# Kernel optimization log

Measured on AMD Instinct MI355X. Metric: run time of the kernel, lower is better.

## Reference

```python
import jax, jax.numpy as jnp
import numpy as np


def setup_inputs() -> dict:
    key = jax.random.key(0)
    ks = jax.random.split(key, 6)
    b, c, h, w = 8, 256, 48, 48
    return {
        "qry_fts": jax.random.normal(ks[0], (b, c, h, w), dtype=jnp.float32),
        "mask_fts": jax.random.normal(ks[1], (b, c, h, w), dtype=jnp.float32),
        "fts": jax.random.normal(ks[2], (b, c, h, w), dtype=jnp.float32),
        "Wq": jax.random.normal(ks[3], (c, c), dtype=jnp.float32) * (1.0 / np.sqrt(c)),
        "Wk": jax.random.normal(ks[4], (c, c), dtype=jnp.float32) * (1.0 / np.sqrt(c)),
        "Wv": jax.random.normal(ks[5], (c, c), dtype=jnp.float32) * (1.0 / np.sqrt(c)),
        "mu": jnp.full((1,), 0.5, dtype=jnp.float32),
    }


def reference(qry_fts, mask_fts, fts, Wq, Wk, Wv, mu):
    b, c, h, w = qry_fts.shape
    # flatten spatial dims to tokens: [b, N, c], N = h*w
    q_tok = qry_fts.reshape(b, c, h * w).transpose(0, 2, 1)
    m_tok = mask_fts.reshape(b, c, h * w).transpose(0, 2, 1)
    f_tok = fts.reshape(b, c, h * w).transpose(0, 2, 1)

    # torch Linear(no bias): y = x @ W^T with W [out,in]
    Q = jnp.einsum("bnc,dc->bnd", q_tok, Wq)
    K1 = jnp.einsum("bnc,dc->bnd", f_tok, Wk)
    K2 = jnp.einsum("bnc,dc->bnd", m_tok, Wk)
    V = jnp.einsum("bnc,dc->bnd", f_tok, Wv)

    A1 = jax.nn.softmax(jnp.einsum("bqd,bkd->bqk", Q, K1), axis=-1)
    A2 = jax.nn.softmax(jnp.einsum("bqd,bkd->bqk", Q, K2), axis=-1)
    A = (A1 * 0.5 + A2 * mu[0]) / (0.5 + mu[0])

    att = jnp.einsum("bqk,bkd->bqd", A, V)  # [b, N, c]
    att = att.reshape(b, h, w, c).transpose(0, 3, 1, 2)
    return qry_fts + att
```

## Files before the change

kernel.cpp:

```cpp
#include <hip/hip_runtime.h>
#include <math.h>

#define BB 8
#define CC 256
#define NTOK 2304
#define NPL 36
#define LOG2E 1.4426950408889634f
#define BIAS2 72.134752f

typedef __attribute__((ext_vector_type(4))) float f32x4;
typedef __attribute__((ext_vector_type(8))) short s16x8;
typedef __attribute__((ext_vector_type(4))) short s16x4;

__device__ inline unsigned short f2bf(float x) {
  unsigned u = __builtin_bit_cast(unsigned, x);
  return (unsigned short)((u + 0x7FFFu + ((u >> 16) & 1u)) >> 16);
}
__device__ inline float bf2f(unsigned short h) {
  return __builtin_bit_cast(float, (unsigned)h << 16);
}
__device__ inline unsigned short f2h(float x) {
  _Float16 h = (_Float16)x;
  return __builtin_bit_cast(unsigned short, h);
}

__device__ inline void async16(void* lds, const void* g) {
  __builtin_amdgcn_global_load_lds(
      (const __attribute__((address_space(1))) unsigned int*)g,
      (__attribute__((address_space(3))) unsigned int*)lds, 16, 0, 0);
}

__global__ __launch_bounds__(256)
void prep_kernel(const float* __restrict__ X0, const float* __restrict__ X1,
                 const float* __restrict__ X2, unsigned short* __restrict__ Y0,
                 unsigned short* __restrict__ Y1, unsigned short* __restrict__ Y2) {
  __shared__ float Ls[64][65];
  const int t = threadIdx.x;
  const int n0 = blockIdx.x * 64, c0 = blockIdx.y * 64;
  const int z = blockIdx.z, src = z >> 3, b = z & 7;
  const float* X = (src == 0) ? X0 : (src == 1) ? X1 : X2;
  unsigned short* Y = (src == 0) ? Y0 : (src == 1) ? Y1 : Y2;
  const float* Xb = X + (size_t)b * CC * NTOK;
  unsigned short* Yb = Y + (size_t)b * CC * NTOK;

  #pragma unroll
  for (int rr = 0; rr < 16; rr++) {
    int cl = rr * 4 + (t >> 6);
    Ls[cl][t & 63] = Xb[(size_t)(c0 + cl) * NTOK + n0 + (t & 63)];
  }
  __syncthreads();
  #pragma unroll
  for (int rr = 0; rr < 8; rr++) {
    int nl = rr * 8 + (t >> 5);
    int cl = (t & 31) * 2;
    unsigned v = (unsigned)f2h(Ls[cl][nl]) | ((unsigned)f2h(Ls[cl + 1][nl]) << 16);
    *(unsigned*)((char*)Yb + ((size_t)(n0 + nl) * CC + c0 + cl) * 2) = v;
  }
}

__global__ __launch_bounds__(256)
void wconv_kernel(const float* __restrict__ Wq, const float* __restrict__ Wk,
                  const float* __restrict__ Wv, unsigned short* __restrict__ Wqh,
                  unsigned short* __restrict__ Wkh, unsigned short* __restrict__ Wvh) {
  const float* src = (blockIdx.y == 0) ? Wq : (blockIdx.y == 1) ? Wk : Wv;
  unsigned short* dst = (blockIdx.y == 0) ? Wqh : (blockIdx.y == 1) ? Wkh : Wvh;
  int gi = (blockIdx.x * 256 + threadIdx.x) * 4;
  f32x4 v = *(const f32x4*)(src + gi);
  s16x4 o;
  #pragma unroll
  for (int i = 0; i < 4; i++) o[i] = (short)f2h(v[i]);
  *(s16x4*)(dst + gi) = o;
}

template<int MODE>
__global__ __launch_bounds__(256, 2)
void gemm_kernel(const unsigned short* __restrict__ Xt, const unsigned short* __restrict__ Wh,
                 unsigned short* __restrict__ Y) {
  __shared__ alignas(16) char smem[32768];

  const int t = threadIdx.x;
  const int w = t >> 6, l = t & 63, g = l >> 4, c = l & 15;
  const int bid = blockIdx.x;
  const int b = bid & 7, nt = bid >> 3;
  const int n0w = nt * 64 + w * 16;
  const size_t bo = (size_t)b * CC * NTOK;

  const char* Xb = (const char*)(Xt + bo);
  const char* Wb = (const char*)Wh;
  char* Yb = (char*)(Y + bo);

  int koff[4], cdst[4];
  #pragma unroll
  for (int j = 0; j < 4; j++) {
    int ck = w + 4 * j;
    int row = ck * 2 + (l >> 5);
    koff[j] = row * 512 + (((l & 31) * 16) ^ ((row & 7) << 4));
    cdst[j] = ck * 1024 + l * 16;
  }
  int kxor[8];
  #pragma unroll
  for (int dc = 0; dc < 8; dc++)
    kxor[dc] = (dc * 64 + g * 16) ^ ((c & 7) << 4);

  s16x8 xa[8];
  #pragma unroll
  for (int dc = 0; dc < 8; dc++)
    xa[dc] = *(const s16x8*)(Xb + (n0w + c) * 512 + dc * 64 + g * 16);

  f32x4 acc[16];

#define STAGE_W(WB, TILE)                                            \
  do {                                                               \
    _Pragma("unroll")                                                \
    for (int j_ = 0; j_ < 4; j_++)                                   \
      async16((WB) + cdst[j_], Wb + (TILE) * 16384 + koff[j_]);      \
  } while (0)

  STAGE_W(smem, 0);
  __syncthreads();

  #pragma unroll
  for (int ph = 0; ph < 8; ph++) {
    char* cur = smem + (ph & 1) * 16384;
    if (ph < 7) STAGE_W(smem + ((ph & 1) ^ 1) * 16384, ph + 1);
    __builtin_amdgcn_s_setprio(1);
    #pragma unroll
    for (int s = 0; s < 2; s++) {
      const char* Kt = cur + (s * 16 + c) * 512;
      f32x4 sx[2] = {(f32x4){0.f, 0.f, 0.f, 0.f}, (f32x4){0.f, 0.f, 0.f, 0.f}};
      #pragma unroll
      for (int dc = 0; dc < 8; dc++) {
        s16x8 wf = *(const s16x8*)(Kt + kxor[dc]);
        sx[dc >> 2] = __builtin_amdgcn_mfma_f32_16x16x32_f16(xa[dc], wf, sx[dc >> 2], 0, 0, 0);
      }
      acc[ph * 2 + s] = sx[0] + sx[1];
    }
    __builtin_amdgcn_s_setprio(0);
    __syncthreads();
  }
#undef STAGE_W

  if (MODE == 0 || MODE == 1) {
    unsigned short* Ws = (unsigned short*)(smem + w * 8192);
    #pragma unroll
    for (int dt = 0; dt < 16; dt++)
      #pragma unroll
      for (int j = 0; j < 4; j++) {
        float v = (MODE == 0) ? acc[dt][j] * LOG2E : acc[dt][j];
        Ws[(g * 4 + j) * 256 + dt * 16 + c] = f2h(v);
      }
    #pragma unroll
    for (int r = 0; r < 16; r++) {
      s16x4 v = *(const s16x4*)&Ws[r * 256 + l * 4];
      *(s16x4*)(Yb + (size_t)(n0w + r) * 512 + l * 8) = v;
    }
  } else {
    unsigned short* Vs = (unsigned short*)(smem + w * 8192);
    #pragma unroll
    for (int dt = 0; dt < 16; dt++) {
      s16x4 pv;
      #pragma unroll
      for (int j = 0; j < 4; j++) pv[j] = (short)f2bf(acc[dt][j]);
      *(s16x4*)&Vs[c * 20 + g * 4] = pv;
      s16x4 vv = *(const s16x4*)&Vs[(l >> 2) * 20 + (l & 3) * 4];
      *(s16x4*)(Yb + (size_t)(dt * 16 + (l >> 2)) * 4608 + (size_t)(n0w + (l & 3) * 4) * 2) = vv;
    }
  }
}

__global__ __launch_bounds__(256, 2)
void attn_kernel(const unsigned short* __restrict__ Qf, const unsigned short* __restrict__ K1,
                 const unsigned short* __restrict__ K2, const unsigned short* __restrict__ Vt,
                 unsigned short* __restrict__ pa1, unsigned short* __restrict__ pa2,
                 float* __restrict__ lb) {
  __shared__ alignas(16) char smem[74752];
  char* const kb0 = smem;
  char* const kb1 = smem + 16384;

  const int t = threadIdx.x;
  const int w = t >> 6, l = t & 63, g = l >> 4, c = l & 15;
  const int bid = blockIdx.x;
  const int b = bid & 7;
  const int r0 = bid >> 3;
  const int qt = r0 % 36, half = r0 / 36;
  const int q0 = qt * 64 + w * 16;
  const size_t bo = (size_t)b * CC * NTOK;

  const char* Qb  = (const char*)(Qf + bo);
  const char* K1b = (const char*)(K1 + bo);
  const char* K2b = (const char*)(K2 + bo);
  const char* Vtb = (const char*)(Vt + bo);

  unsigned short* const Pe0 = (unsigned short*)(smem + 65536 + w * 2304);
  unsigned short* const Pe1 = Pe0 + 384;
  unsigned short* const Pod = Pe0 + 768;

  int koff[2], voff[2], cdst[2];
  #pragma unroll
  for (int j = 0; j < 2; j++) {
    int ck = w + 4 * j;
    int tok = ck * 2 + (l >> 5);
    koff[j] = tok * 512 + (((l & 31) * 16) ^ ((tok & 7) << 4));
    voff[j] = (ck * 32 + (l >> 1)) * 4608 + (((l & 1) ^ ((l >> 3) & 1)) << 4);
    cdst[j] = ck * 1024 + l * 16;
  }

  int kxor[8];
  #pragma unroll
  for (int dc = 0; dc < 8; dc++)
    kxor[dc] = (dc * 64 + g * 16) ^ ((c & 7) << 4);

  s16x8 qf[8];
  #pragma unroll
  for (int dc = 0; dc < 8; dc++)
    qf[dc] = *(const s16x8*)(Qb + (q0 + c) * 512 + dc * 64 + g * 16);

  f32x4 a1[16], a2[16];
  #pragma unroll
  for (int dt = 0; dt < 16; dt++) {
    a1[dt] = (f32x4){0.f, 0.f, 0.f, 0.f};
    a2[dt] = (f32x4){0.f, 0.f, 0.f, 0.f};
  }
  float lr1[4] = {0.f, 0.f, 0.f, 0.f};
  float lr2[4] = {0.f, 0.f, 0.f, 0.f};

#define STAGE_K(KB, TILE)                                                  \
  do {                                                                     \
    _Pragma("unroll")                                                      \
    for (int pp_ = 0; pp_ < 2; pp_++) {                                    \
      const char* ks_ = (pp_ ? K2b : K1b) + (size_t)(TILE) * 8192;         \
      async16((KB) + pp_ * 8192 + cdst[0], ks_ + koff[0]);                 \
      async16((KB) + pp_ * 8192 + cdst[1], ks_ + koff[1]);                 \
    }                                                                      \
  } while (0)

#define STAGE_V(VB, PAIR)                                                  \
  do {                                                                     \
    _Pragma("unroll")                                                      \
    for (int h_ = 0; h_ < 2; h_++) {                                       \
      const char* vs_ = Vtb + (PAIR) * 64 + h_ * 32;                       \
      async16((VB) + h_ * 8192 + cdst[0], vs_ + voff[0]);                  \
      async16((VB) + h_ * 8192 + cdst[1], vs_ + voff[1]);                  \
    }                                                                      \
  } while (0)

  const int tb = half * 72;
  const int pb = half * 36;

  STAGE_K(kb0, tb);
  STAGE_V(smem + 32768, pb);
  __syncthreads();

  for (int p = 0; p < NPL; p++) {
    char* vcur = smem + 32768 + (p & 1) * 16384;
    char* vnxt = smem + 32768 + ((p & 1) ^ 1) * 16384;

    STAGE_K(kb1, tb + 2 * p + 1);
    #pragma unroll
    for (int pp = 0; pp < 2; pp++) {
      const char* Kt = kb0 + pp * 8192 + c * 512;
      f32x4 sx[2] = {(f32x4){0.f, 0.f, 0.f, 0.f}, (f32x4){0.f, 0.f, 0.f, 0.f}};
      __builtin_amdgcn_s_setprio(1);
      #pragma unroll
      for (int dc = 0; dc < 8; dc++) {
        s16x8 kf = *(const s16x8*)(Kt + kxor[dc]);
        sx[dc >> 2] = __builtin_amdgcn_mfma_f32_16x16x32_f16(qf[dc], kf, sx[dc >> 2], 0, 0, 0);
      }
      __builtin_amdgcn_s_setprio(0);
      f32x4 s = sx[0] + sx[1];
      float* lr = pp ? lr2 : lr1;
      unsigned short* Pe = pp ? Pe1 : Pe0;
      #pragma unroll
      for (int j = 0; j < 4; j++) {
        float pv = exp2f(s[j] - BIAS2);
        lr[j] += pv;
        Pe[(g * 4 + j) * 24 + c] = f2bf(pv);
      }
    }
    __syncthreads();

    if (p + 1 < NPL) {
      STAGE_K(kb0, tb + 2 * p + 2);
      STAGE_V(vnxt, pb + p + 1);
    }
    s16x8 pa0, pa1r;
    #pragma unroll
    for (int pp = 0; pp < 2; pp++) {
      const char* Kt = kb1 + pp * 8192 + c * 512;
      f32x4 sx[2] = {(f32x4){0.f, 0.f, 0.f, 0.f}, (f32x4){0.f, 0.f, 0.f, 0.f}};
      __builtin_amdgcn_s_setprio(1);
      #pragma unroll
      for (int dc = 0; dc < 8; dc++) {
        s16x8 kf = *(const s16x8*)(Kt + kxor[dc]);
        sx[dc >> 2] = __builtin_amdgcn_mfma_f32_16x16x32_f16(qf[dc], kf, sx[dc >> 2], 0, 0, 0);
      }
      __builtin_amdgcn_s_setprio(0);
      f32x4 s = sx[0] + sx[1];
      float* lr = pp ? lr2 : lr1;
      #pragma unroll
      for (int j = 0; j < 4; j++) {
        float pv = exp2f(s[j] - BIAS2);
        lr[j] += pv;
        Pod[(g * 4 + j) * 24 + c] = f2bf(pv);
      }
      const unsigned short* src = ((g < 2) ? (pp ? Pe1 : Pe0) : Pod) + c * 24 + (g & 1) * 8;
      s16x8 v = *(const s16x8*)src;
      if (pp == 0) pa0 = v; else pa1r = v;
    }
    {
      const char* vbase = vcur + ((g >= 2) ? 8192 : 0) + c * 32 +
                          ((((g & 1) ^ ((c >> 2) & 1))) << 4);
      __builtin_amdgcn_s_setprio(1);
      #pragma unroll
      for (int dt = 0; dt < 16; dt++) {
        s16x8 vf = *(const s16x8*)(vbase + dt * 512);
        a1[dt] = __builtin_amdgcn_mfma_f32_16x16x32_bf16(pa0, vf, a1[dt], 0, 0, 0);
        a2[dt] = __builtin_amdgcn_mfma_f32_16x16x32_bf16(pa1r, vf, a2[dt], 0, 0, 0);
      }
      __builtin_amdgcn_s_setprio(0);
    }
    __syncthreads();
  }
#undef STAGE_K
#undef STAGE_V

  #pragma unroll
  for (int j = 0; j < 4; j++) {
    #pragma unroll
    for (int off = 1; off < 16; off <<= 1) {
      lr1[j] += __shfl_xor(lr1[j], off);
      lr2[j] += __shfl_xor(lr2[j], off);
    }
  }
  const int pqidx = (half * 8 + b) * 36 + qt;
  if (c == 0) {
    #pragma unroll
    for (int j = 0; j < 4; j++) {
      int row = w * 16 + g * 4 + j;
      lb[pqidx * 64 + row] = lr1[j];
      lb[36864 + pqidx * 64 + row] = lr2[j];
    }
  }

  unsigned short* const pb1 = pa1 + (size_t)pqidx * 16384;
  unsigned short* const pb2 = pa2 + (size_t)pqidx * 16384;
  float* Ws = (float*)(smem + w * 4352);
  const int q = l & 15, ds = l >> 4;
  #pragma unroll
  for (int ch = 0; ch < 4; ch++) {
    #pragma unroll
    for (int pth = 0; pth < 2; pth++) {
      const f32x4* ap = pth ? a2 : a1;
      unsigned short* pdst = pth ? pb2 : pb1;
      #pragma unroll
      for (int dtp = 0; dtp < 4; dtp++) {
        const int dt = ch * 4 + dtp;
        #pragma unroll
        for (int j = 0; j < 4; j++)
          Ws[(g * 4 + j) * 68 + dtp * 16 + c] = ap[dt][j];
      }
      #pragma unroll
      for (int i = 0; i < 16; i++) {
        int d = ch * 64 + i * 4 + ds;
        pdst[d * 64 + w * 16 + q] = f2bf(Ws[q * 68 + i * 4 + ds]);
      }
      __builtin_amdgcn_s_barrier();
    }
  }
}

__global__ __launch_bounds__(256)
void combine_kernel(const unsigned short* __restrict__ pa1, const unsigned short* __restrict__ pa2,
                    const float* __restrict__ lb, const float* __restrict__ qry,
                    const float* __restrict__ mup, float* __restrict__ out) {
  const int bid = blockIdx.x;
  const int b = bid & 7, qt = bid >> 3;
  const int t = threadIdx.x;
  const int q = t & 63, dr = t >> 6;
  const size_t bo = (size_t)b * CC * NTOK;
  const int q0 = qt * 64;

  const int i0 = (0 * 8 + b) * 36 + qt;
  const int i1 = (1 * 8 + b) * 36 + qt;
  float l1 = lb[i0 * 64 + q] + lb[i1 * 64 + q];
  float l2 = lb[36864 + i0 * 64 + q] + lb[36864 + i1 * 64 + q];
  const float mu = mup[0];
  const float w1 = 0.5f / (0.5f + mu) / l1;
  const float w2 = mu / (0.5f + mu) / l2;

  const unsigned short* p10 = pa1 + (size_t)i0 * 16384;
  const unsigned short* p11 = pa1 + (size_t)i1 * 16384;
  const unsigned short* p20 = pa2 + (size_t)i0 * 16384;
  const unsigned short* p21 = pa2 + (size_t)i1 * 16384;

  #pragma unroll
  for (int i = 0; i < 64; i++) {
    int d = dr * 64 + i;
    int off = d * 64 + q;
    float av1 = bf2f(p10[off]) + bf2f(p11[off]);
    float av2 = bf2f(p20[off]) + bf2f(p21[off]);
    size_t gi = bo + (size_t)d * NTOK + q0 + q;
    out[gi] = qry[gi] + av1 * w1 + av2 * w2;
  }
}

extern "C" void kernel_launch(void* const* d_in, const int* in_sizes, int n_in,
                              void* d_out, int out_size, void* d_ws, size_t ws_size,
                              hipStream_t stream) {
  const float* qry  = (const float*)d_in[0];
  const float* mask = (const float*)d_in[1];
  const float* fts  = (const float*)d_in[2];
  const float* Wq   = (const float*)d_in[3];
  const float* Wk   = (const float*)d_in[4];
  const float* Wv   = (const float*)d_in[5];
  const float* mu   = (const float*)d_in[6];
  float* out = (float*)d_out;

  const size_t SZ = (size_t)BB * CC * NTOK;
  unsigned short* base = (unsigned short*)d_ws;
  unsigned short* PA1 = base;
  unsigned short* PA2 = base + 9437184;
  float*          LB  = (float*)(base + 18874368);
  unsigned short* Xtq = base;
  unsigned short* Xtm = base + SZ;
  unsigned short* Xtf = base + 2 * SZ;
  unsigned short* Qw  = base + 19169280;
  unsigned short* K1w = Qw + SZ;
  unsigned short* K2w = Qw + 2 * SZ;
  unsigned short* Vtw = Qw + 3 * SZ;
  unsigned short* Wqh = Qw + 4 * SZ;
  unsigned short* Wkh = Wqh + CC * CC;
  unsigned short* Wvh = Wkh + CC * CC;

  prep_kernel<<<dim3(NTOK / 64, CC / 64, 24), 256, 0, stream>>>(qry, mask, fts, Xtq, Xtm, Xtf);
  wconv_kernel<<<dim3(64, 3), 256, 0, stream>>>(Wq, Wk, Wv, Wqh, Wkh, Wvh);

  const int GG = BB * (NTOK / 64);
  gemm_kernel<0><<<GG, 256, 0, stream>>>(Xtq, Wqh, Qw);
  gemm_kernel<1><<<GG, 256, 0, stream>>>(Xtf, Wkh, K1w);
  gemm_kernel<1><<<GG, 256, 0, stream>>>(Xtm, Wkh, K2w);
  gemm_kernel<2><<<GG, 256, 0, stream>>>(Xtf, Wvh, Vtw);

  attn_kernel<<<2 * GG, 256, 0, stream>>>(Qw, K1w, K2w, Vtw, PA1, PA2, LB);
  combine_kernel<<<GG, 256, 0, stream>>>(PA1, PA2, LB, qry, mu, out);
}
```

Before: 247.1 us.

## Split attention warps by softmax path and double query rows per warp

```diff
diff --git a/kernel.cpp b/kernel.cpp
--- a/kernel.cpp
+++ b/kernel.cpp
@@ -173,17 +173,18 @@
                  const unsigned short* __restrict__ K2, const unsigned short* __restrict__ Vt,
                  unsigned short* __restrict__ pa1, unsigned short* __restrict__ pa2,
                  float* __restrict__ lb) {
-  __shared__ alignas(16) char smem[74752];
+  __shared__ alignas(16) char smem[77824];
   char* const kb0 = smem;
   char* const kb1 = smem + 16384;
 
   const int t = threadIdx.x;
   const int w = t >> 6, l = t & 63, g = l >> 4, c = l & 15;
+  const int path = w >> 1, qs = w & 1;
   const int bid = blockIdx.x;
   const int b = bid & 7;
   const int r0 = bid >> 3;
   const int qt = r0 % 36, half = r0 / 36;
-  const int q0 = qt * 64 + w * 16;
+  const int q0 = qt * 64 + qs * 32;
   const size_t bo = (size_t)b * CC * NTOK;
 
   const char* Qb  = (const char*)(Qf + bo);
@@ -191,9 +192,8 @@
   const char* K2b = (const char*)(K2 + bo);
   const char* Vtb = (const char*)(Vt + bo);
 
-  unsigned short* const Pe0 = (unsigned short*)(smem + 65536 + w * 2304);
-  unsigned short* const Pe1 = Pe0 + 384;
-  unsigned short* const Pod = Pe0 + 768;
+  unsigned short* const Pe  = (unsigned short*)(smem + 65536 + w * 3072);
+  unsigned short* const Pod = Pe + 768;
 
   int koff[2], voff[2], cdst[2];
   #pragma unroll
@@ -210,19 +210,20 @@
   for (int dc = 0; dc < 8; dc++)
     kxor[dc] = (dc * 64 + g * 16) ^ ((c & 7) << 4);
 
-  s16x8 qf[8];
-  #pragma unroll
-  for (int dc = 0; dc < 8; dc++)
-    qf[dc] = *(const s16x8*)(Qb + (q0 + c) * 512 + dc * 64 + g * 16);
-
-  f32x4 a1[16], a2[16];
+  s16x8 qf[2][8];
+  #pragma unroll
+  for (int st = 0; st < 2; st++)
+    #pragma unroll
+    for (int dc = 0; dc < 8; dc++)
+      qf[st][dc] = *(const s16x8*)(Qb + (q0 + st * 16 + c) * 512 + dc * 64 + g * 16);
+
+  f32x4 a0[16], a1r[16];
   #pragma unroll
   for (int dt = 0; dt < 16; dt++) {
-    a1[dt] = (f32x4){0.f, 0.f, 0.f, 0.f};
-    a2[dt] = (f32x4){0.f, 0.f, 0.f, 0.f};
-  }
-  float lr1[4] = {0.f, 0.f, 0.f, 0.f};
-  float lr2[4] = {0.f, 0.f, 0.f, 0.f};
+    a0[dt]  = (f32x4){0.f, 0.f, 0.f, 0.f};
+    a1r[dt] = (f32x4){0.f, 0.f, 0.f, 0.f};
+  }
+  float lr[2][4] = {{0.f, 0.f, 0.f, 0.f}, {0.f, 0.f, 0.f, 0.f}};
 
 #define STAGE_K(KB, TILE)                                                  \
   do {                                                                     \
@@ -256,25 +257,26 @@
     char* vnxt = smem + 32768 + ((p & 1) ^ 1) * 16384;
 
     STAGE_K(kb1, tb + 2 * p + 1);
-    #pragma unroll
-    for (int pp = 0; pp < 2; pp++) {
-      const char* Kt = kb0 + pp * 8192 + c * 512;
-      f32x4 sx[2] = {(f32x4){0.f, 0.f, 0.f, 0.f}, (f32x4){0.f, 0.f, 0.f, 0.f}};
+    {
+      const char* Kt = kb0 + path * 8192 + c * 512;
+      f32x4 s0 = (f32x4){0.f, 0.f, 0.f, 0.f};
+      f32x4 s1 = (f32x4){0.f, 0.f, 0.f, 0.f};
       __builtin_amdgcn_s_setprio(1);
       #pragma unroll
       for (int dc = 0; dc < 8; dc++) {
         s16x8 kf = *(const s16x8*)(Kt + kxor[dc]);
-        sx[dc >> 2] = __builtin_amdgcn_mfma_f32_16x16x32_f16(qf[dc], kf, sx[dc >> 2], 0, 0, 0);
+        s0 = __builtin_amdgcn_mfma_f32_16x16x32_f16(qf[0][dc], kf, s0, 0, 0, 0);
+        s1 = __builtin_amdgcn_mfma_f32_16x16x32_f16(qf[1][dc], kf, s1, 0, 0, 0);
       }
       __builtin_amdgcn_s_setprio(0);
-      f32x4 s = sx[0] + sx[1];
-      float* lr = pp ? lr2 : lr1;
-      unsigned short* Pe = pp ? Pe1 : Pe0;
       #pragma unroll
       for (int j = 0; j < 4; j++) {
-        float pv = exp2f(s[j] - BIAS2);
-        lr[j] += pv;
+        float pv = exp2f(s0[j] - BIAS2);
+        lr[0][j] += pv;
         Pe[(g * 4 + j) * 24 + c] = f2bf(pv);
+        float pw = exp2f(s1[j] - BIAS2);
+        lr[1][j] += pw;
+        Pe[(16 + g * 4 + j) * 24 + c] = f2bf(pw);
       }
     }
     __syncthreads();
@@ -283,39 +285,39 @@
       STAGE_K(kb0, tb + 2 * p + 2);
       STAGE_V(vnxt, pb + p + 1);
     }
-    s16x8 pa0, pa1r;
-    #pragma unroll
-    for (int pp = 0; pp < 2; pp++) {
-      const char* Kt = kb1 + pp * 8192 + c * 512;
-      f32x4 sx[2] = {(f32x4){0.f, 0.f, 0.f, 0.f}, (f32x4){0.f, 0.f, 0.f, 0.f}};
+    {
+      const char* Kt = kb1 + path * 8192 + c * 512;
+      f32x4 s0 = (f32x4){0.f, 0.f, 0.f, 0.f};
+      f32x4 s1 = (f32x4){0.f, 0.f, 0.f, 0.f};
       __builtin_amdgcn_s_setprio(1);
       #pragma unroll
       for (int dc = 0; dc < 8; dc++) {
         s16x8 kf = *(const s16x8*)(Kt + kxor[dc]);
-        sx[dc >> 2] = __builtin_amdgcn_mfma_f32_16x16x32_f16(qf[dc], kf, sx[dc >> 2], 0, 0, 0);
+        s0 = __builtin_amdgcn_mfma_f32_16x16x32_f16(qf[0][dc], kf, s0, 0, 0, 0);
+        s1 = __builtin_amdgcn_mfma_f32_16x16x32_f16(qf[1][dc], kf, s1, 0, 0, 0);
       }
       __builtin_amdgcn_s_setprio(0);
-      f32x4 s = sx[0] + sx[1];
-      float* lr = pp ? lr2 : lr1;
       #pragma unroll
       for (int j = 0; j < 4; j++) {
-        float pv = exp2f(s[j] - BIAS2);
-        lr[j] += pv;
+        float pv = exp2f(s0[j] - BIAS2);
+        lr[0][j] += pv;
         Pod[(g * 4 + j) * 24 + c] = f2bf(pv);
-      }
-      const unsigned short* src = ((g < 2) ? (pp ? Pe1 : Pe0) : Pod) + c * 24 + (g & 1) * 8;
-      s16x8 v = *(const s16x8*)src;
-      if (pp == 0) pa0 = v; else pa1r = v;
+        float pw = exp2f(s1[j] - BIAS2);
+        lr[1][j] += pw;
+        Pod[(16 + g * 4 + j) * 24 + c] = f2bf(pw);
+      }
     }
     {
+      s16x8 pa0 = *(const s16x8*)(((g < 2) ? Pe : Pod) + (c) * 24 + (g & 1) * 8);
+      s16x8 pa1 = *(const s16x8*)(((g < 2) ? Pe : Pod) + (16 + c) * 24 + (g & 1) * 8);
       const char* vbase = vcur + ((g >= 2) ? 8192 : 0) + c * 32 +
                           ((((g & 1) ^ ((c >> 2) & 1))) << 4);
       __builtin_amdgcn_s_setprio(1);
       #pragma unroll
       for (int dt = 0; dt < 16; dt++) {
         s16x8 vf = *(const s16x8*)(vbase + dt * 512);
-        a1[dt] = __builtin_amdgcn_mfma_f32_16x16x32_bf16(pa0, vf, a1[dt], 0, 0, 0);
-        a2[dt] = __builtin_amdgcn_mfma_f32_16x16x32_bf16(pa1r, vf, a2[dt], 0, 0, 0);
+        a0[dt]  = __builtin_amdgcn_mfma_f32_16x16x32_bf16(pa0, vf, a0[dt], 0, 0, 0);
+        a1r[dt] = __builtin_amdgcn_mfma_f32_16x16x32_bf16(pa1, vf, a1r[dt], 0, 0, 0);
       }
       __builtin_amdgcn_s_setprio(0);
     }
@@ -325,33 +327,30 @@
 #undef STAGE_V
 
   #pragma unroll
-  for (int j = 0; j < 4; j++) {
-    #pragma unroll
-    for (int off = 1; off < 16; off <<= 1) {
-      lr1[j] += __shfl_xor(lr1[j], off);
-      lr2[j] += __shfl_xor(lr2[j], off);
-    }
-  }
+  for (int st = 0; st < 2; st++)
+    #pragma unroll
+    for (int j = 0; j < 4; j++) {
+      #pragma unroll
+      for (int off = 1; off < 16; off <<= 1)
+        lr[st][j] += __shfl_xor(lr[st][j], off);
+    }
   const int pqidx = (half * 8 + b) * 36 + qt;
   if (c == 0) {
     #pragma unroll
-    for (int j = 0; j < 4; j++) {
-      int row = w * 16 + g * 4 + j;
-      lb[pqidx * 64 + row] = lr1[j];
-      lb[36864 + pqidx * 64 + row] = lr2[j];
-    }
-  }
-
-  unsigned short* const pb1 = pa1 + (size_t)pqidx * 16384;
-  unsigned short* const pb2 = pa2 + (size_t)pqidx * 16384;
+    for (int st = 0; st < 2; st++)
+      #pragma unroll
+      for (int j = 0; j < 4; j++)
+        lb[path * 36864 + pqidx * 64 + qs * 32 + st * 16 + g * 4 + j] = lr[st][j];
+  }
+
+  unsigned short* const pdst = (path ? pa2 : pa1) + (size_t)pqidx * 16384;
   float* Ws = (float*)(smem + w * 4352);
   const int q = l & 15, ds = l >> 4;
   #pragma unroll
-  for (int ch = 0; ch < 4; ch++) {
-    #pragma unroll
-    for (int pth = 0; pth < 2; pth++) {
-      const f32x4* ap = pth ? a2 : a1;
-      unsigned short* pdst = pth ? pb2 : pb1;
+  for (int st = 0; st < 2; st++) {
+    const f32x4* ap = st ? a1r : a0;
+    #pragma unroll
+    for (int ch = 0; ch < 4; ch++) {
       #pragma unroll
       for (int dtp = 0; dtp < 4; dtp++) {
         const int dt = ch * 4 + dtp;
@@ -362,9 +361,8 @@
       #pragma unroll
       for (int i = 0; i < 16; i++) {
         int d = ch * 64 + i * 4 + ds;
-        pdst[d * 64 + w * 16 + q] = f2bf(Ws[q * 68 + i * 4 + ds]);
-      }
-      __builtin_amdgcn_s_barrier();
+        pdst[d * 64 + qs * 32 + st * 16 + q] = f2bf(Ws[q * 68 + i * 4 + ds]);
+      }
     }
   }
 }
```

Result: no change. 246.9 us (-0.1%).
